# Optimization experiments

Hardware: AMD Instinct MI355X
Metric: run time of the kernel (lower is better)

## Reference

```python
import jax, jax.numpy as jnp
import numpy as np


def setup_inputs() -> dict:
    key = jax.random.key(0)
    k1, k2, k3 = jax.random.split(key, 3)
    B, Cin, D, H, W = 16, 3, 16, 128, 128
    Cout, K = 24, 3
    x = jax.random.normal(k1, (B, Cin, D, H, W), dtype=jnp.float32)
    # torch Conv3d default init scale ~ 1/sqrt(fan_in); use small scale for stability
    fan_in = Cin * K * K * K
    conv_weight = jax.random.normal(k2, (Cout, Cin, K, K, K), dtype=jnp.float32) / np.sqrt(fan_in)
    conv_bias = jax.random.normal(k3, (Cout,), dtype=jnp.float32) * 0.01
    return {"x": x, "conv_weight": conv_weight, "conv_bias": conv_bias}


def reference(x, conv_weight, conv_bias):
    # Conv3d, stride=1, padding=0, dilation=1, groups=1
    y = jax.lax.conv_general_dilated(
        x, conv_weight,
        window_strides=(1, 1, 1),
        padding='VALID',
        dimension_numbers=('NCDHW', 'OIDHW', 'NCDHW'),
    )
    y = y + conv_bias[None, :, None, None, None]  # [B, Cout, D', H', W']
    y = jnp.min(y, axis=2)                        # min over depth -> [B, Cout, H', W']
    return jax.nn.softmax(y, axis=1)              # softmax over channels
```

## Files before the change

kernel.cpp:

```cpp
#include <hip/hip_runtime.h>
#include <math.h>

#define CIN 3
#define DIN 16
#define HIN 128
#define WIN 128
#define COUT 24
#define HOUT 126
#define DOUT 14
#define HW (HIN * WIN)

using f16x8 = __attribute__((ext_vector_type(8))) _Float16;
using f32x4 = __attribute__((ext_vector_type(4))) float;

#define ROWSTRIDE 18
#define SLOT_HALVES (162 * ROWSTRIDE)
#define TAIL 96
#define LDS_HALVES (2 * SLOT_HALVES + TAIL)

__global__ __launch_bounds__(256) void conv3d_min_softmax_mfma(
    const float* __restrict__ x,
    const float* __restrict__ wgt,
    const float* __restrict__ bias,
    float* __restrict__ out)
{
    __shared__ _Float16 imX[LDS_HALVES];

    const int tid  = threadIdx.x;
    const int wv   = tid >> 6;
    const int lane = tid & 63;
    const int cl   = lane & 15;
    const int kg   = lane >> 4;
    const bool has11 = (tid < 32);

    const int wchunk = blockIdx.x;
    const int band   = blockIdx.y;
    const int b      = blockIdx.z;
    const int w0 = (wchunk < 7) ? wchunk * 16 : 110;
    const int h0 = (band   < 7) ? band   * 16 : 110;

    const float* xb = x + (size_t)b * (CIN * DIN * HW);

    for (int i = 2 * SLOT_HALVES + tid; i < LDS_HALVES; i += 256)
        imX[i] = (_Float16)0.f;

    f16x8 bw[3][2];
    #pragma unroll
    for (int kd = 0; kd < 3; ++kd)
      #pragma unroll
      for (int hf = 0; hf < 2; ++hf)
        #pragma unroll
        for (int j = 0; j < 8; ++j) {
          int k  = kg * 8 + j;
          int co = hf * 16 + cl;
          float wvv = 0.f;
          if (k < 27 && co < 24) {
            int kh = k / 9, rem = k - kh * 9, ci = rem / 3, kw = rem - ci * 3;
            wvv = wgt[((co * 3 + ci) * 3 + kd) * 9 + kh * 3 + kw];
          }
          bw[kd][hf][j] = (_Float16)wvv;
        }

    const float bias0 = bias[cl];
    const float bias1 = (cl < 8) ? bias[16 + cl] : 0.f;

    int goff[11];
    int lidx[11];
    #pragma unroll
    for (int it = 0; it < 11; ++it) {
      int e = tid + it * 256;
      int ec = (e < 2592) ? e : 0;
      int hrow = ec / 144, e2 = ec - hrow * 144;
      int ci   = e2 / 48,  e3 = e2 - ci * 48;
      int kw   = e3 >> 4,  px = e3 & 15;
      goff[it] = (ci * DIN) * HW + (h0 + hrow) * WIN + (w0 + kw + px);
      lidx[it] = (hrow * 9 + ci * 3 + kw) * ROWSTRIDE + px;
    }

    int rbase[4];
    #pragma unroll
    for (int t = 0; t < 4; ++t)
      rbase[t] = ((wv * 4 + t) * 9 + kg * 8) * ROWSTRIDE + cl;

    #pragma unroll 1
    for (int s = 0; s < 2; ++s) {
      #pragma unroll
      for (int it = 0; it < 10; ++it)
        imX[s * SLOT_HALVES + lidx[it]] = (_Float16)xb[goff[it] + s * HW];
      if (has11)
        imX[s * SLOT_HALVES + lidx[10]] = (_Float16)xb[goff[10] + s * HW];
    }
    __syncthreads();

    f16x8 A0[4], A1[4], A2[4];
    #pragma unroll
    for (int t = 0; t < 4; ++t)
      #pragma unroll
      for (int j = 0; j < 8; ++j) {
        A0[t][j] = imX[0 * SLOT_HALVES + rbase[t] + j * ROWSTRIDE];
        A1[t][j] = imX[1 * SLOT_HALVES + rbase[t] + j * ROWSTRIDE];
      }
    __syncthreads();

    #pragma unroll
    for (int it = 0; it < 10; ++it)
      imX[0 * SLOT_HALVES + lidx[it]] = (_Float16)xb[goff[it] + 2 * HW];
    if (has11)
      imX[0 * SLOT_HALVES + lidx[10]] = (_Float16)xb[goff[10] + 2 * HW];
    __syncthreads();

    #pragma unroll
    for (int t = 0; t < 4; ++t)
      #pragma unroll
      for (int j = 0; j < 8; ++j)
        A2[t][j] = imX[0 * SLOT_HALVES + rbase[t] + j * ROWSTRIDE];

    float mn[4][2][4];
    #pragma unroll
    for (int t = 0; t < 4; ++t)
      #pragma unroll
      for (int hf = 0; hf < 2; ++hf)
        #pragma unroll
        for (int j = 0; j < 4; ++j) mn[t][hf][j] = 3.4e38f;

    #pragma unroll 1
    for (int dp = 0; dp < DOUT; ++dp) {
      const bool more = (dp < DOUT - 1);

      float stash[11];
      if (more) {
        #pragma unroll
        for (int it = 0; it < 10; ++it)
          stash[it] = xb[goff[it] + (dp + 3) * HW];
        if (has11)
          stash[10] = xb[goff[10] + (dp + 3) * HW];
      }

      #pragma unroll
      for (int t = 0; t < 4; ++t) {
        f32x4 z = {0.f, 0.f, 0.f, 0.f};
        f32x4 acc0 = __builtin_amdgcn_mfma_f32_16x16x32_f16(A0[t], bw[0][0], z, 0, 0, 0);
        f32x4 acc1 = __builtin_amdgcn_mfma_f32_16x16x32_f16(A0[t], bw[0][1], z, 0, 0, 0);
        acc0 = __builtin_amdgcn_mfma_f32_16x16x32_f16(A1[t], bw[1][0], acc0, 0, 0, 0);
        acc1 = __builtin_amdgcn_mfma_f32_16x16x32_f16(A1[t], bw[1][1], acc1, 0, 0, 0);
        acc0 = __builtin_amdgcn_mfma_f32_16x16x32_f16(A2[t], bw[2][0], acc0, 0, 0, 0);
        acc1 = __builtin_amdgcn_mfma_f32_16x16x32_f16(A2[t], bw[2][1], acc1, 0, 0, 0);
        #pragma unroll
        for (int j = 0; j < 4; ++j) {
          mn[t][0][j] = fminf(mn[t][0][j], acc0[j]);
          mn[t][1][j] = fminf(mn[t][1][j], acc1[j]);
        }
      }

      if (more) {
        const int sb = ((dp + 1) & 1) * SLOT_HALVES;
        #pragma unroll
        for (int it = 0; it < 10; ++it)
          imX[sb + lidx[it]] = (_Float16)stash[it];
        if (has11)
          imX[sb + lidx[10]] = (_Float16)stash[10];
        __syncthreads();
        #pragma unroll
        for (int t = 0; t < 4; ++t) { A0[t] = A1[t]; A1[t] = A2[t]; }
        #pragma unroll
        for (int t = 0; t < 4; ++t)
          #pragma unroll
          for (int j = 0; j < 8; ++j)
            A2[t][j] = imX[sb + rbase[t] + j * ROWSTRIDE];
      }
    }

    float* ob = out + (size_t)b * COUT * HOUT * HOUT;
    #pragma unroll
    for (int t = 0; t < 4; ++t) {
      const int h = h0 + wv * 4 + t;
      #pragma unroll
      for (int j = 0; j < 4; ++j) {
        float v0 = mn[t][0][j] + bias0;
        float v1 = (cl < 8) ? (mn[t][1][j] + bias1) : -3.4e38f;
        float mx = fmaxf(v0, v1);
        #pragma unroll
        for (int msk = 1; msk < 16; msk <<= 1)
          mx = fmaxf(mx, __shfl_xor(mx, msk));
        float e0 = __expf(v0 - mx);
        float e1 = (cl < 8) ? __expf(v1 - mx) : 0.f;
        float sm = e0 + e1;
        #pragma unroll
        for (int msk = 1; msk < 16; msk <<= 1)
          sm += __shfl_xor(sm, msk);
        float r = 1.f / sm;
        const int w = w0 + kg * 4 + j;
        ob[((size_t)cl * HOUT + h) * HOUT + w] = e0 * r;
        if (cl < 8)
          ob[((size_t)(16 + cl) * HOUT + h) * HOUT + w] = e1 * r;
      }
    }
}

extern "C" void kernel_launch(void* const* d_in, const int* in_sizes, int n_in,
                              void* d_out, int out_size, void* d_ws, size_t ws_size,
                              hipStream_t stream) {
    const float* x    = (const float*)d_in[0];
    const float* wgt  = (const float*)d_in[1];
    const float* bias = (const float*)d_in[2];
    float* out        = (float*)d_out;

    dim3 grid(8, 8, 16);
    dim3 block(256);
    conv3d_min_softmax_mfma<<<grid, block, 0, stream>>>(x, wgt, bias, out);
}
```

Before: 84.33 us.

## Double-buffer global stash registers to prefetch two depth slices ahead

Global loads for the next input depth slice now go into two alternating register stash arrays, issued two iterations ahead instead of one. The depth loop is unrolled by two so the stash roles swap statically. The __syncthreads is replaced by an explicit lgkmcnt wait plus a raw s_barrier, so the barrier does not also wait on the outstanding global loads. This hides more global-memory latency behind the MFMA work, at the cost of about 11 extra live VGPRs per thread.

Measured after the change: 126.9 us. 50.5% more time.

```diff
diff --git a/kernel.cpp b/kernel.cpp
--- a/kernel.cpp
+++ b/kernel.cpp
@@ -82,6 +82,18 @@
     for (int t = 0; t < 4; ++t)
       rbase[t] = ((wv * 4 + t) * 9 + kg * 8) * ROWSTRIDE + cl;
 
+#define STAGE_LOAD(SL, s)                                   \
+    { _Pragma("unroll")                                     \
+      for (int it = 0; it < 10; ++it)                       \
+        SL[it] = xb[goff[it] + (s) * HW];                   \
+      if (has11) SL[10] = xb[goff[10] + (s) * HW]; }
+
+#define STAGE_WRITE(SW, sb)                                 \
+    { _Pragma("unroll")                                     \
+      for (int it = 0; it < 10; ++it)                       \
+        imX[(sb) + lidx[it]] = (_Float16)SW[it];            \
+      if (has11) imX[(sb) + lidx[10]] = (_Float16)SW[10]; }
+
     #pragma unroll 1
     for (int s = 0; s < 2; ++s) {
       #pragma unroll
@@ -115,6 +127,9 @@
       for (int j = 0; j < 8; ++j)
         A2[t][j] = imX[0 * SLOT_HALVES + rbase[t] + j * ROWSTRIDE];
 
+    float stashA[11], stashB[11];
+    STAGE_LOAD(stashA, 3);
+
     float mn[4][2][4];
     #pragma unroll
     for (int t = 0; t < 4; ++t)
@@ -123,51 +138,43 @@
         #pragma unroll
         for (int j = 0; j < 4; ++j) mn[t][hf][j] = 3.4e38f;
 
+#define DP_BODY(dp, SW, SL)                                              \
+    {                                                                    \
+      if ((dp) < 12) STAGE_LOAD(SL, (dp) + 4);                           \
+      _Pragma("unroll")                                                  \
+      for (int t = 0; t < 4; ++t) {                                      \
+        f32x4 z = {0.f, 0.f, 0.f, 0.f};                                  \
+        f32x4 acc0 = __builtin_amdgcn_mfma_f32_16x16x32_f16(A0[t], bw[0][0], z, 0, 0, 0); \
+        f32x4 acc1 = __builtin_amdgcn_mfma_f32_16x16x32_f16(A0[t], bw[0][1], z, 0, 0, 0); \
+        acc0 = __builtin_amdgcn_mfma_f32_16x16x32_f16(A1[t], bw[1][0], acc0, 0, 0, 0);    \
+        acc1 = __builtin_amdgcn_mfma_f32_16x16x32_f16(A1[t], bw[1][1], acc1, 0, 0, 0);    \
+        acc0 = __builtin_amdgcn_mfma_f32_16x16x32_f16(A2[t], bw[2][0], acc0, 0, 0, 0);    \
+        acc1 = __builtin_amdgcn_mfma_f32_16x16x32_f16(A2[t], bw[2][1], acc1, 0, 0, 0);    \
+        _Pragma("unroll")                                                \
+        for (int j = 0; j < 4; ++j) {                                    \
+          mn[t][0][j] = fminf(mn[t][0][j], acc0[j]);                     \
+          mn[t][1][j] = fminf(mn[t][1][j], acc1[j]);                     \
+        }                                                                \
+      }                                                                  \
+      if ((dp) < 13) {                                                   \
+        const int sb = (((dp) + 1) & 1) * SLOT_HALVES;                   \
+        STAGE_WRITE(SW, sb);                                             \
+        asm volatile("s_waitcnt lgkmcnt(0)" ::: "memory");               \
+        __builtin_amdgcn_s_barrier();                                    \
+        _Pragma("unroll")                                                \
+        for (int t = 0; t < 4; ++t) { A0[t] = A1[t]; A1[t] = A2[t]; }    \
+        _Pragma("unroll")                                                \
+        for (int t = 0; t < 4; ++t)                                      \
+          _Pragma("unroll")                                              \
+          for (int j = 0; j < 8; ++j)                                    \
+            A2[t][j] = imX[sb + rbase[t] + j * ROWSTRIDE];               \
+      }                                                                  \
+    }
+
     #pragma unroll 1
-    for (int dp = 0; dp < DOUT; ++dp) {
-      const bool more = (dp < DOUT - 1);
-
-      float stash[11];
-      if (more) {
-        #pragma unroll
-        for (int it = 0; it < 10; ++it)
-          stash[it] = xb[goff[it] + (dp + 3) * HW];
-        if (has11)
-          stash[10] = xb[goff[10] + (dp + 3) * HW];
-      }
-
-      #pragma unroll
-      for (int t = 0; t < 4; ++t) {
-        f32x4 z = {0.f, 0.f, 0.f, 0.f};
-        f32x4 acc0 = __builtin_amdgcn_mfma_f32_16x16x32_f16(A0[t], bw[0][0], z, 0, 0, 0);
-        f32x4 acc1 = __builtin_amdgcn_mfma_f32_16x16x32_f16(A0[t], bw[0][1], z, 0, 0, 0);
-        acc0 = __builtin_amdgcn_mfma_f32_16x16x32_f16(A1[t], bw[1][0], acc0, 0, 0, 0);
-        acc1 = __builtin_amdgcn_mfma_f32_16x16x32_f16(A1[t], bw[1][1], acc1, 0, 0, 0);
-        acc0 = __builtin_amdgcn_mfma_f32_16x16x32_f16(A2[t], bw[2][0], acc0, 0, 0, 0);
-        acc1 = __builtin_amdgcn_mfma_f32_16x16x32_f16(A2[t], bw[2][1], acc1, 0, 0, 0);
-        #pragma unroll
-        for (int j = 0; j < 4; ++j) {
-          mn[t][0][j] = fminf(mn[t][0][j], acc0[j]);
-          mn[t][1][j] = fminf(mn[t][1][j], acc1[j]);
-        }
-      }
-
-      if (more) {
-        const int sb = ((dp + 1) & 1) * SLOT_HALVES;
-        #pragma unroll
-        for (int it = 0; it < 10; ++it)
-          imX[sb + lidx[it]] = (_Float16)stash[it];
-        if (has11)
-          imX[sb + lidx[10]] = (_Float16)stash[10];
-        __syncthreads();
-        #pragma unroll
-        for (int t = 0; t < 4; ++t) { A0[t] = A1[t]; A1[t] = A2[t]; }
-        #pragma unroll
-        for (int t = 0; t < 4; ++t)
-          #pragma unroll
-          for (int j = 0; j < 8; ++j)
-            A2[t][j] = imX[sb + rbase[t] + j * ROWSTRIDE];
-      }
+    for (int dpe = 0; dpe < DOUT; dpe += 2) {
+      DP_BODY(dpe,     stashA, stashB);
+      DP_BODY(dpe + 1, stashB, stashA);
     }
 
     float* ob = out + (size_t)b * COUT * HOUT * HOUT;
```
